# Kernel tuning notes

Measured on AMD Instinct MI355X. Metric: run time of the kernel, lower is better.

The kernel has to match this reference:

```python
import jax, jax.numpy as jnp
import numpy as np

THRESHOLD = 1.0   # spiking threshold (also used for reset detection)
BETA = 0.95       # reservoir membrane decay
N = 2048          # reservoir_size


def _heaviside(x):
    # snntorch Heaviside: (x > 0).float()
    return (x > 0).astype(x.dtype)


def setup_inputs() -> dict:
    key = jax.random.key(0)
    k1, k2, k3 = jax.random.split(key, 3)
    B, T = 32, 500
    x = jax.random.normal(k1, (B, T, 1), dtype=jnp.float32)
    # recurrent connectivity matrix loaded from .npy in the original; random here
    W = jax.random.normal(k2, (N, N), dtype=jnp.float32) / jnp.sqrt(jnp.float32(N))
    # nn.Linear default bias init: U(-1/sqrt(N), 1/sqrt(N))
    bound = 1.0 / np.sqrt(N)
    b = jax.random.uniform(k3, (N,), dtype=jnp.float32, minval=-bound, maxval=bound)
    return {"x": x, "W": W, "b": b}


def reference(x, W, b):
    """RLeaky reservoir with reset_mechanism='zero', reset_delay=True.
    Per step (snntorch RLeaky semantics):
      reset   = heaviside(mem_prev - threshold)            (detached)
      base    = beta*mem_prev + input + W @ spk_prev + b
      mem_new = base - reset*base                          ('zero' reset)
      spk_new = heaviside(mem_new - threshold)
    Input current = scalar x_t broadcast across all N neurons.
    """
    B = x.shape[0]
    Wt = W.T  # (N, N), spk @ W.T == Linear(spk)

    def step(carry, x_t):
        spk, mem = carry  # each (B, N)
        reset = _heaviside(mem - THRESHOLD)
        base = BETA * mem + x_t + spk @ Wt + b  # x_t: (B,1) broadcasts over N
        mem_new = base * (1.0 - reset)
        spk_new = _heaviside(mem_new - THRESHOLD)
        return (spk_new, mem_new), (spk_new, mem_new)

    init = (jnp.zeros((B, N), x.dtype), jnp.zeros((B, N), x.dtype))
    xs = jnp.swapaxes(x, 0, 1)  # (T, B, 1)
    _, (spk_rec, mem_rec) = jax.lax.scan(step, init, xs)
    avg_firing_rate = spk_rec.mean()
    return avg_firing_rate, spk_rec, mem_rec
```

## Files before the change

kernel.cpp:

```cpp
#include <hip/hip_runtime.h>
#include <hip/hip_cooperative_groups.h>

namespace cg = cooperative_groups;

#define NN 2048
#define NB 32
#define NT 500
#define WGS 1024
#define NWG 256


__launch_bounds__(WGS, 4)
__global__ void reservoir_kernel(const float* __restrict__ x,
                                 const float* __restrict__ W,
                                 const float* __restrict__ bias,
                                 float* __restrict__ out,
                                 void* __restrict__ wsv)
{
    cg::grid_group grid = cg::this_grid();

    __shared__ unsigned int lbits[NN];
    __shared__ float lpart[8][8][32];
    __shared__ float lout[2][NB][9];
    __shared__ int   lcnt[4];

    unsigned long long* data64 = (unsigned long long*)wsv;
    unsigned int* ep  = (unsigned int*)((char*)wsv + 16384);
    float* xT         = (float*)((char*)wsv + 20480);
    int*   wgpart     = (int*)((char*)wsv + 86016);

    const int wg = blockIdx.x;
    const int t  = threadIdx.x;
    const int i0 = wg * 8;

    {
        int g = wg * WGS + t;
        if (g < 1024) {
            __hip_atomic_store(&data64[g], 0ull,
                               __ATOMIC_RELAXED, __HIP_MEMORY_SCOPE_AGENT);
            __hip_atomic_store(&ep[g], 0u,
                               __ATOMIC_RELAXED, __HIP_MEMORY_SCOPE_AGENT);
        }
        for (; g < NT * NB; g += NWG * WGS)
            xT[g] = x[(size_t)(g & 31) * NT + (g >> 5)];
    }

    const int rh = t >> 8;
    const int jh = (t >> 5) & 7;
    const int b  = t & 31;

    const float4* __restrict__ wr0 = (const float4*)(W + (size_t)(i0 + 2 * rh    ) * NN) + jh * 64;
    const float4* __restrict__ wr1 = (const float4*)(W + (size_t)(i0 + 2 * rh + 1) * NN) + jh * 64;

    const int cil = t >> 5;
    const int cb  = t & 31;
    const float biasv = (t < 256) ? bias[i0 + cil] : 0.0f;
    float mem = 0.0f;
    int   cnt = 0;

    float* spk_rec = out + 1;
    float* mem_rec = out + 1 + (size_t)NT * NB * NN;

    grid.sync();

    for (int step = 0; step < NT; ++step) {
        const int cur = step & 1;

        const float xv = (t < 256) ? xT[step * NB + cb] : 0.0f;

        {
            for (;;) {
                unsigned int e = __hip_atomic_load(&ep[t], __ATOMIC_RELAXED,
                                                   __HIP_MEMORY_SCOPE_AGENT);
                if (e >= (unsigned int)step) break;
                __builtin_amdgcn_s_sleep(1);
            }
            unsigned long long v =
                __hip_atomic_load(&data64[(size_t)cur * 1024 + t],
                                  __ATOMIC_RELAXED, __HIP_MEMORY_SCOPE_AGENT);
            *(unsigned long long*)&lbits[2 * t] = v;
        }
        __syncthreads();

        float c0 = 0.0f, c1 = 0.0f;
        const uint4* bp = ((const uint4*)lbits) + jh * 64;
        #pragma unroll 4
        for (int jj = 0; jj < 64; ++jj) {
            const float4 w0 = wr0[jj];
            const float4 w1 = wr1[jj];
            const uint4  bu = bp[jj];
            float s;
            s = (float)((bu.x >> b) & 1u); c0 = fmaf(w0.x, s, c0); c1 = fmaf(w1.x, s, c1);
            s = (float)((bu.y >> b) & 1u); c0 = fmaf(w0.y, s, c0); c1 = fmaf(w1.y, s, c1);
            s = (float)((bu.z >> b) & 1u); c0 = fmaf(w0.z, s, c0); c1 = fmaf(w1.z, s, c1);
            s = (float)((bu.w >> b) & 1u); c0 = fmaf(w0.w, s, c0); c1 = fmaf(w1.w, s, c1);
        }
        lpart[jh][2 * rh    ][b] = c0;
        lpart[jh][2 * rh + 1][b] = c1;
        __syncthreads();

        if (t < 256) {
            float d = lpart[0][cil][cb];
            #pragma unroll
            for (int k = 1; k < 8; ++k) d += lpart[k][cil][cb];

            const float sp = (float)((lbits[i0 + cil] >> cb) & 1u);

            float base = 0.95f * mem + xv + d + biasv;
            float nm   = base * (1.0f - sp);
            float ns   = (nm > 1.0f) ? 1.0f : 0.0f;
            mem = nm;
            cnt += (int)ns;

            unsigned long long bal = __ballot(ns > 0.5f);
            const int l  = t & 63;
            const int w2 = t >> 6;
            if (l == 0)
                __hip_atomic_store(&data64[(size_t)(1 - cur) * 1024 + 4 * wg + w2],
                                   bal, __ATOMIC_RELAXED, __HIP_MEMORY_SCOPE_AGENT);
            asm volatile("s_waitcnt vmcnt(0)" ::: "memory");
            if (l == 0)
                __hip_atomic_store(&ep[4 * wg + w2], (unsigned int)(step + 1),
                                   __ATOMIC_RELAXED, __HIP_MEMORY_SCOPE_AGENT);

            lout[0][cb][cil] = ns;
            lout[1][cb][cil] = nm;
        }
        __syncthreads();

        if (t < 512) {
            const int arr = t >> 8;
            const int r2  = t & 255;
            const int bb  = r2 >> 3;
            const int il  = r2 & 7;
            size_t o = ((size_t)step * NB + bb) * (size_t)NN + i0 + il;
            if (arr == 0) __builtin_nontemporal_store(lout[0][bb][il], &spk_rec[o]);
            else          __builtin_nontemporal_store(lout[1][bb][il], &mem_rec[o]);
        }
    }

    #pragma unroll
    for (int d2 = 1; d2 < 64; d2 <<= 1) cnt += __shfl_xor(cnt, d2, 64);
    if ((t & 63) == 0 && t < 256) lcnt[t >> 6] = cnt;
    __syncthreads();
    if (t == 0) wgpart[wg] = lcnt[0] + lcnt[1] + lcnt[2] + lcnt[3];
    grid.sync();
    if (wg == 0) {
        int ps = (t < NWG) ? wgpart[t] : 0;
        #pragma unroll
        for (int d2 = 1; d2 < 64; d2 <<= 1) ps += __shfl_xor(ps, d2, 64);
        if ((t & 63) == 0 && t < 256) lcnt[t >> 6] = ps;
        __syncthreads();
        if (t == 0) {
            long long s2 = (long long)lcnt[0] + lcnt[1] + lcnt[2] + lcnt[3];
            out[0] = (float)((double)s2 / (double)((long long)NT * NB * NN));
        }
    }
}

extern "C" void kernel_launch(void* const* d_in, const int* in_sizes, int n_in,
                              void* d_out, int out_size, void* d_ws, size_t ws_size,
                              hipStream_t stream) {
    const float* x    = (const float*)d_in[0];
    const float* W    = (const float*)d_in[1];
    const float* bias = (const float*)d_in[2];
    float* out = (float*)d_out;
    void*  ws  = d_ws;

    void* args[] = { (void*)&x, (void*)&W, (void*)&bias, (void*)&out, (void*)&ws };
    hipLaunchCooperativeKernel((const void*)reservoir_kernel,
                               dim3(NWG), dim3(WGS), args, 0, stream);
}
```

Before: 9.788 ms.

## Replace per-slot epoch flags with striped atomic arrival counters for step sync

Swaps the per-wave epoch flags, which every thread polled (1024 polls per workgroup per step), for eight cache-line-strided arrival counters, one set per ping-pong parity. Only four threads per workgroup poll the counters before a barrier. Spike bitmasks are now written and read with inline-asm global loads and stores using sc0 sc1 cache bits, meant to give coherence without atomic ops. This cuts polling traffic across the grid but concentrates 1024 fetch-add atomics per step on four addresses, which risks contention at the L2 atomic units.

```diff
diff --git a/kernel.cpp b/kernel.cpp
--- a/kernel.cpp
+++ b/kernel.cpp
@@ -9,6 +9,19 @@
 #define WGS 1024
 #define NWG 256
 
+
+__device__ __forceinline__ unsigned long long load_coh8(const void* p) {
+    unsigned long long v;
+    asm volatile("global_load_dwordx2 %0, %1, off sc0 sc1\n\t"
+                 "s_waitcnt vmcnt(0)"
+                 : "=&v"(v) : "v"(p) : "memory");
+    return v;
+}
+
+__device__ __forceinline__ void store_coh8(void* p, unsigned long long v) {
+    asm volatile("global_store_dwordx2 %0, %1, off sc0 sc1"
+                 :: "v"(p), "v"(v) : "memory");
+}
 
 __launch_bounds__(WGS, 4)
 __global__ void reservoir_kernel(const float* __restrict__ x,
@@ -24,26 +37,20 @@
     __shared__ float lout[2][NB][9];
     __shared__ int   lcnt[4];
 
-    unsigned long long* data64 = (unsigned long long*)wsv;
-    unsigned int* ep  = (unsigned int*)((char*)wsv + 16384);
-    float* xT         = (float*)((char*)wsv + 20480);
-    int*   wgpart     = (int*)((char*)wsv + 86016);
+    unsigned long long* buf = (unsigned long long*)wsv;
+    unsigned int* cnt       = (unsigned int*)((char*)wsv + 16384);
+    float* xT               = (float*)((char*)wsv + 17408);
+    int*   wgpart           = (int*)((char*)wsv + 81408);
 
     const int wg = blockIdx.x;
     const int t  = threadIdx.x;
     const int i0 = wg * 8;
 
-    {
-        int g = wg * WGS + t;
-        if (g < 1024) {
-            __hip_atomic_store(&data64[g], 0ull,
-                               __ATOMIC_RELAXED, __HIP_MEMORY_SCOPE_AGENT);
-            __hip_atomic_store(&ep[g], 0u,
-                               __ATOMIC_RELAXED, __HIP_MEMORY_SCOPE_AGENT);
-        }
-        for (; g < NT * NB; g += NWG * WGS)
-            xT[g] = x[(size_t)(g & 31) * NT + (g >> 5)];
-    }
+    if (wg == 0 && t < 8)
+        __hip_atomic_store(&cnt[t * 32], 0u,
+                           __ATOMIC_RELAXED, __HIP_MEMORY_SCOPE_AGENT);
+    for (int g = wg * WGS + t; g < NT * NB; g += NWG * WGS)
+        xT[g] = x[(size_t)(g & 31) * NT + (g >> 5)];
 
     const int rh = t >> 8;
     const int jh = (t >> 5) & 7;
@@ -56,30 +63,35 @@
     const int cb  = t & 31;
     const float biasv = (t < 256) ? bias[i0 + cil] : 0.0f;
     float mem = 0.0f;
-    int   cnt = 0;
+    int   scount = 0;
 
     float* spk_rec = out + 1;
     float* mem_rec = out + 1 + (size_t)NT * NB * NN;
 
     grid.sync();
 
+    unsigned int tgt0 = 0, tgt1 = 0;
+
     for (int step = 0; step < NT; ++step) {
-        const int cur = step & 1;
+        const int pcur = step & 1;
 
-        const float xv = (t < 256) ? xT[step * NB + cb] : 0.0f;
+        if (step == 0) {
+            ((uint2*)lbits)[t] = make_uint2(0u, 0u);
+        } else {
+            if (pcur) tgt1 += 256; else tgt0 += 256;
+            const unsigned int tg = pcur ? tgt1 : tgt0;
+            if (t < 4) {
+                while (__hip_atomic_load(&cnt[(pcur * 4 + t) * 32], __ATOMIC_RELAXED,
+                                         __HIP_MEMORY_SCOPE_AGENT) < tg)
+                    __builtin_amdgcn_s_sleep(1);
+            }
+            __syncthreads();
 
-        {
-            for (;;) {
-                unsigned int e = __hip_atomic_load(&ep[t], __ATOMIC_RELAXED,
-                                                   __HIP_MEMORY_SCOPE_AGENT);
-                if (e >= (unsigned int)step) break;
-                __builtin_amdgcn_s_sleep(1);
-            }
             unsigned long long v =
-                __hip_atomic_load(&data64[(size_t)cur * 1024 + t],
-                                  __ATOMIC_RELAXED, __HIP_MEMORY_SCOPE_AGENT);
+                load_coh8((const char*)(buf + (size_t)pcur * 1024) + 8 * t);
             *(unsigned long long*)&lbits[2 * t] = v;
         }
+        const float xv = (t < 256) ? xT[step * NB + cb] : 0.0f;
         __syncthreads();
 
         float c0 = 0.0f, c1 = 0.0f;
@@ -110,18 +122,18 @@
             float nm   = base * (1.0f - sp);
             float ns   = (nm > 1.0f) ? 1.0f : 0.0f;
             mem = nm;
-            cnt += (int)ns;
+            scount += (int)ns;
 
             unsigned long long bal = __ballot(ns > 0.5f);
             const int l  = t & 63;
             const int w2 = t >> 6;
+            const int pnxt = pcur ^ 1;
             if (l == 0)
-                __hip_atomic_store(&data64[(size_t)(1 - cur) * 1024 + 4 * wg + w2],
-                                   bal, __ATOMIC_RELAXED, __HIP_MEMORY_SCOPE_AGENT);
+                store_coh8((char*)(buf + (size_t)pnxt * 1024) + 8 * (4 * wg + w2), bal);
             asm volatile("s_waitcnt vmcnt(0)" ::: "memory");
             if (l == 0)
-                __hip_atomic_store(&ep[4 * wg + w2], (unsigned int)(step + 1),
-                                   __ATOMIC_RELAXED, __HIP_MEMORY_SCOPE_AGENT);
+                __hip_atomic_fetch_add(&cnt[(pnxt * 4 + w2) * 32], 1u,
+                                       __ATOMIC_RELAXED, __HIP_MEMORY_SCOPE_AGENT);
 
             lout[0][cb][cil] = ns;
             lout[1][cb][cil] = nm;
@@ -140,8 +152,8 @@
     }
 
     #pragma unroll
-    for (int d2 = 1; d2 < 64; d2 <<= 1) cnt += __shfl_xor(cnt, d2, 64);
-    if ((t & 63) == 0 && t < 256) lcnt[t >> 6] = cnt;
+    for (int d2 = 1; d2 < 64; d2 <<= 1) scount += __shfl_xor(scount, d2, 64);
+    if ((t & 63) == 0 && t < 256) lcnt[t >> 6] = scount;
     __syncthreads();
     if (t == 0) wgpart[wg] = lcnt[0] + lcnt[1] + lcnt[2] + lcnt[3];
     grid.sync();
```

Result: slower. 13.92 ms (+42.2%).
